# Optimization experiments

Measured on AMD Instinct MI355X. Metric: run time of the kernel, lower is better.

## Reference

```python
import math
import jax, jax.numpy as jnp
import numpy as np

B, N, D_IN, D_OUT = 8, 2048, 768, 768

def setup_inputs() -> dict:
    key = jax.random.key(0)
    k1, k2, k3 = jax.random.split(key, 3)
    x = jax.random.normal(k1, (B, N, D_IN), dtype=jnp.float32)
    W_qkv = jax.random.normal(k2, (D_IN, 3 * D_OUT), dtype=jnp.float32) * (1.0 / math.sqrt(D_IN))
    b_qkv = jax.random.normal(k3, (3 * D_OUT,), dtype=jnp.float32) * 0.02
    return {"x": x, "W_qkv": W_qkv, "b_qkv": b_qkv}

def reference(x, W_qkv, b_qkv):
    d_out = D_OUT
    # fused QKV projection: [B, N, 3*d_out]
    qkv = jnp.einsum('bnd,de->bne', x, W_qkv) + b_qkv
    q = qkv[:, :, :d_out]
    k = qkv[:, :, d_out:2 * d_out]
    v = qkv[:, :, 2 * d_out:3 * d_out]
    scale = 1.0 / math.sqrt(d_out)
    # scores: [B, N, N]
    scores = jnp.einsum('bqd,bkd->bqk', q, k) * scale
    attn = jax.nn.softmax(scores, axis=-1)
    # context: [B, N, d_out]
    context = jnp.einsum('bqk,bkd->bqd', attn, v)
    return context
```

## Files before the change

### kernel.cpp

```cpp
#include <hip/hip_runtime.h>
#include <hip/hip_bf16.h>

typedef __attribute__((ext_vector_type(8))) short short8;
typedef __attribute__((ext_vector_type(4))) float floatx4;

#define BATCH 8
#define SEQ 2048
#define DMODEL 768
#define NQKV 2304
#define SCALE 0.03608439182435161f

__device__ __forceinline__ ushort f2bf(float f) {
    union { float f; uint u; } in; in.f = f;
    uint u = in.u;
    return (ushort)((u + 0x7FFFu + ((u >> 16) & 1u)) >> 16);
}
__device__ __forceinline__ float bf2f(ushort h) {
    union { uint u; float f; } o; o.u = ((uint)h) << 16;
    return o.f;
}

__device__ __forceinline__ void async_copy16(void* lds_uniform, const void* gaddr) {
    __builtin_amdgcn_global_load_lds(
        (const __attribute__((address_space(1))) void*)gaddr,
        (__attribute__((address_space(3))) void*)lds_uniform,
        16, 0, 0);
}

#define BARRIER() asm volatile("s_barrier" ::: "memory")
#define LGKM0()   do { asm volatile("s_waitcnt lgkmcnt(0)" ::: "memory"); \
                       __builtin_amdgcn_sched_barrier(0); } while (0)
#define LGKM_HINT() asm volatile("s_waitcnt lgkmcnt(8)" ::: "memory")
#define VMCNT(n)  asm volatile("s_waitcnt vmcnt(" #n ")" ::: "memory")

template<int MODE, int KT>
__global__ __launch_bounds__(512, 2) void gemm8(
    const ushort* __restrict__ A, const ushort* __restrict__ B,
    const float* __restrict__ bias,
    void* __restrict__ out0, void* __restrict__ out1, void* __restrict__ out2,
    int lda, int ldb)
{
    extern __shared__ __align__(16) ushort lds[];
    const int tid  = threadIdx.x;
    const int w    = tid >> 6, lane = tid & 63;
    const int wr   = w >> 2,  wc   = w & 3;
    const int lr   = lane & 15, kg = lane >> 4;
    const int srow = lane >> 3;
    const int scc  = (lane & 7) ^ srow;

    const int m0 = blockIdx.x * 256, n0 = blockIdx.y * 256;
    const ushort* Abase;
    const ushort* Bbase;
    if (MODE == 0) {
        Abase = A + (size_t)m0 * lda;
        Bbase = B + (size_t)n0 * ldb;
    } else {
        const int b = blockIdx.z;
        Abase = A + ((size_t)(b * SEQ + m0)) * lda;
        Bbase = B + ((size_t)(b * SEQ + n0)) * ldb;
    }

    const ushort* At[2] = { lds,         lds + 32768 };
    const ushort* Bt[2] = { lds + 16384, lds + 49152 };

    #define STG(tile, mat, half) do { if ((tile) < KT) {                          \
        ushort* sb_ = lds + (((tile) & 1) ? 32768 : 0) + ((mat) ? 16384 : 0);     \
        const ushort* g_ = (mat) ? Bbase : Abase;                                 \
        const size_t ld_ = (mat) ? (size_t)ldb : (size_t)lda;                     \
        const int k0_ = (tile) << 6;                                              \
        _Pragma("unroll")                                                         \
        for (int t_ = 0; t_ < 2; ++t_) {                                          \
            const int c8_ = (mat) ? ((w & 3) + ((w >> 2) << 3) + (t_ << 4) + ((half) << 2)) \
                                  : (w + (t_ << 4) + ((half) << 3));              \
            const int row_ = (c8_ << 3) + srow;                                   \
            async_copy16(sb_ + c8_ * 512, g_ + (size_t)row_ * ld_ + k0_ + scc * 8); \
        } } } while (0)

    short8 af[4][2], bf[4][2];
    floatx4 acc[8][4] = {};

    #define LDFRAG(tp, row, c) \
        (*reinterpret_cast<const short8*>(&(tp)[((row) << 6) + ((((c) ^ ((row) & 7))) << 3)]))

    #define READ_A(bufi, mh) do {                                                 \
        _Pragma("unroll") for (int mf_ = 0; mf_ < 4; ++mf_)                       \
        _Pragma("unroll") for (int kk_ = 0; kk_ < 2; ++kk_)                       \
            af[mf_][kk_] = LDFRAG(At[bufi], wr * 128 + ((mh) * 4 + mf_) * 16 + lr, kk_ * 4 + kg); \
    } while (0)
    #define READ_B(bufi, nh) do {                                                 \
        _Pragma("unroll") for (int nf_ = 0; nf_ < 2; ++nf_)                       \
        _Pragma("unroll") for (int kk_ = 0; kk_ < 2; ++kk_)                       \
            bf[(nh) * 2 + nf_][kk_] = LDFRAG(Bt[bufi], wc * 64 + ((nh) * 2 + nf_) * 16 + lr, kk_ * 4 + kg); \
    } while (0)
    #define MFMA_Q(mh, nh) do {                                                   \
        __builtin_amdgcn_s_setprio(1);                                            \
        _Pragma("unroll") for (int mf_ = 0; mf_ < 4; ++mf_)                       \
        _Pragma("unroll") for (int nf_ = 0; nf_ < 2; ++nf_)                       \
        _Pragma("unroll") for (int kk_ = 0; kk_ < 2; ++kk_)                       \
            acc[(mh) * 4 + mf_][(nh) * 2 + nf_] = __builtin_amdgcn_mfma_f32_16x16x32_bf16( \
                af[mf_][kk_], bf[(nh) * 2 + nf_][kk_], acc[(mh) * 4 + mf_][(nh) * 2 + nf_], 0, 0, 0); \
        __builtin_amdgcn_s_setprio(0);                                            \
    } while (0)

    STG(0, 0, 0); STG(0, 1, 0); STG(0, 1, 1); STG(0, 0, 1);
    STG(1, 0, 0); STG(1, 1, 0); STG(1, 1, 1);
    VMCNT(6);
    BARRIER();

    #pragma unroll 1
    for (int it = 0; it < KT / 2; ++it) {
        const int t = 2 * it;
        const bool lastit = (it == KT / 2 - 1);
        READ_A(0, 0); READ_B(0, 0);
        STG(t + 1, 0, 1);
        LGKM_HINT();
        BARRIER(); LGKM0();
        MFMA_Q(0, 0);
        BARRIER();
        READ_B(0, 1);
        STG(t + 2, 0, 0);
        BARRIER(); LGKM0();
        MFMA_Q(0, 1);
        BARRIER();
        READ_A(0, 1);
        STG(t + 2, 1, 0);
        BARRIER(); LGKM0();
        MFMA_Q(1, 0);
        BARRIER();
        STG(t + 2, 1, 1);
        BARRIER();
        MFMA_Q(1, 1);
        if (lastit) { VMCNT(0); } else { VMCNT(6); }
        BARRIER();
        READ_A(1, 0); READ_B(1, 0);
        STG(t + 2, 0, 1);
        LGKM_HINT();
        BARRIER(); LGKM0();
        MFMA_Q(0, 0);
        BARRIER();
        READ_B(1, 1);
        STG(t + 3, 0, 0);
        BARRIER(); LGKM0();
        MFMA_Q(0, 1);
        BARRIER();
        READ_A(1, 1);
        STG(t + 3, 1, 0);
        BARRIER(); LGKM0();
        MFMA_Q(1, 0);
        BARRIER();
        STG(t + 3, 1, 1);
        BARRIER();
        MFMA_Q(1, 1);
        VMCNT(6);
        BARRIER();
    }

    const int mrow = m0 + wr * 128;
    const int ncol = n0 + wc * 64;

    if (MODE == 0 && blockIdx.y >= 6) {
        ushort* Vt = (ushort*)out2;
        const int bIdx = m0 >> 11;
        const int ns0  = m0 & 2047;
        #pragma unroll
        for (int nf = 0; nf < 4; ++nf) {
            const int e = ncol + nf * 16 + lr;
            const int d = e - 2 * DMODEL;
            const float bv = bias[e];
            ushort* vrow = Vt + ((size_t)bIdx * DMODEL + d) * SEQ + ns0;
            #pragma unroll
            for (int a = 0; a < 8; ++a) {
                const floatx4 v = acc[a][nf];
                uint2 u;
                u.x = (uint)f2bf(v[0] + bv) | ((uint)f2bf(v[1] + bv) << 16);
                u.y = (uint)f2bf(v[2] + bv) | ((uint)f2bf(v[3] + bv) << 16);
                *reinterpret_cast<uint2*>(vrow + wr * 128 + a * 16 + kg * 4) = u;
            }
        }
    } else {
        float* scr = reinterpret_cast<float*>(reinterpret_cast<char*>(lds) + (size_t)w * 9216);
        #pragma unroll
        for (int mh = 0; mh < 2; ++mh) {
            #pragma unroll
            for (int np = 0; np < 2; ++np) {
                #pragma unroll
                for (int mf = 0; mf < 4; ++mf)
                    #pragma unroll
                    for (int nf2 = 0; nf2 < 2; ++nf2) {
                        const floatx4 v = acc[mh * 4 + mf][np * 2 + nf2];
                        #pragma unroll
                        for (int r = 0; r < 4; ++r)
                            scr[(mf * 16 + kg * 4 + r) * 36 + nf2 * 16 + lr] = v[r];
                    }
                asm volatile("s_waitcnt lgkmcnt(0)" ::: "memory");
                __builtin_amdgcn_sched_barrier(0);

                const int c8 = (lane & 3) * 8;
                const int e0 = ncol + np * 32 + c8;
                ushort* dst; int ec; float mul;
                float bs[8] = {0, 0, 0, 0, 0, 0, 0, 0};
                if (MODE == 0) {
                    const bool isQ = e0 < DMODEL;
                    dst = isQ ? (ushort*)out0 : (ushort*)out1;
                    ec  = isQ ? e0 : e0 - DMODEL;
                    mul = isQ ? SCALE : 1.0f;
                    const float4 b0 = *reinterpret_cast<const float4*>(&bias[e0]);
                    const float4 b1 = *reinterpret_cast<const float4*>(&bias[e0 + 4]);
                    bs[0] = b0.x * mul; bs[1] = b0.y * mul;
                    bs[2] = b0.z * mul; bs[3] = b0.w * mul;
                    bs[4] = b1.x * mul; bs[5] = b1.y * mul;
                    bs[6] = b1.z * mul; bs[7] = b1.w * mul;
                } else {
                    dst = (ushort*)out0 + (size_t)blockIdx.z * SEQ * SEQ;
                    ec = e0; mul = 1.0f;
                }
                const size_t ostride = (MODE == 0) ? (size_t)DMODEL : (size_t)SEQ;
                #pragma unroll
                for (int p = 0; p < 4; ++p) {
                    const int row = p * 16 + (lane >> 2);
                    const float4 lo = *reinterpret_cast<const float4*>(&scr[row * 36 + c8]);
                    const float4 hi = *reinterpret_cast<const float4*>(&scr[row * 36 + c8 + 4]);
                    short8 o;
                    o[0] = (short)f2bf(lo.x * mul + bs[0]);
                    o[1] = (short)f2bf(lo.y * mul + bs[1]);
                    o[2] = (short)f2bf(lo.z * mul + bs[2]);
                    o[3] = (short)f2bf(lo.w * mul + bs[3]);
                    o[4] = (short)f2bf(hi.x * mul + bs[4]);
                    o[5] = (short)f2bf(hi.y * mul + bs[5]);
                    o[6] = (short)f2bf(hi.z * mul + bs[6]);
                    o[7] = (short)f2bf(hi.w * mul + bs[7]);
                    *reinterpret_cast<short8*>(
                        &dst[(size_t)(mrow + mh * 64 + row) * ostride + ec]) = o;
                }
                asm volatile("s_waitcnt lgkmcnt(0)" ::: "memory");
                __builtin_amdgcn_sched_barrier(0);
            }
        }
    }
    #undef STG
    #undef LDFRAG
    #undef READ_A
    #undef READ_B
    #undef MFMA_Q
}

__global__ __launch_bounds__(512, 4) void pv128(
    const ushort* __restrict__ P, const ushort* __restrict__ V,
    float* __restrict__ Out)
{
    extern __shared__ __align__(16) ushort lds[];
    const int tid  = threadIdx.x;
    const int w    = tid >> 6, lane = tid & 63;
    const int wr   = w >> 2,  wc   = w & 3;
    const int lr   = lane & 15, kg = lane >> 4;
    const int srow = lane >> 3;
    const int scc  = (lane & 7) ^ srow;

    const int m0 = blockIdx.x * 128, n0 = blockIdx.y * 192;
    const int b  = blockIdx.z;
    const ushort* Abase = P + (size_t)b * SEQ * SEQ + (size_t)m0 * SEQ;
    const ushort* Bbase = V + (size_t)b * DMODEL * SEQ + (size_t)n0 * SEQ;

    const ushort* At[2] = { lds,         lds + 8192 };
    const ushort* Bt[2] = { lds + 16384, lds + 28672 };
    const int KT = 32;

    #define STG_A(tile, half) do { if ((tile) < KT) {                             \
        ushort* sb_ = lds + (((tile) & 1) ? 8192 : 0);                            \
        const int k0_ = (tile) << 6;                                              \
        const int c8_ = (w & 3) + ((w >> 2) << 3) + ((half) << 2);                \
        const int row_ = (c8_ << 3) + srow;                                       \
        async_copy16(sb_ + c8_ * 512, Abase + (size_t)row_ * SEQ + k0_ + scc * 8); \
    } } while (0)
    #define STG_B0(tile) do { if ((tile) < KT) {                                  \
        ushort* sb_ = lds + 16384 + (((tile) & 1) ? 12288 : 0);                   \
        const int k0_ = (tile) << 6;                                              \
        _Pragma("unroll")                                                         \
        for (int t_ = 0; t_ < 2; ++t_) {                                          \
            const int idx_ = w * 2 + t_;                                          \
            const int c8_ = (idx_ >> 2) * 6 + (idx_ & 3);                         \
            const int row_ = (c8_ << 3) + srow;                                   \
            async_copy16(sb_ + c8_ * 512, Bbase + (size_t)row_ * SEQ + k0_ + scc * 8); \
        } } } while (0)
    #define STG_B1(tile) do { if ((tile) < KT) {                                  \
        ushort* sb_ = lds + 16384 + (((tile) & 1) ? 12288 : 0);                   \
        const int k0_ = (tile) << 6;                                              \
        const int c8_ = (w >> 1) * 6 + 4 + (w & 1);                               \
        const int row_ = (c8_ << 3) + srow;                                       \
        async_copy16(sb_ + c8_ * 512, Bbase + (size_t)row_ * SEQ + k0_ + scc * 8); \
    } } while (0)

    short8 af[2][2], bf[3][2];
    floatx4 acc[4][3] = {};

    #define LDFRAG(tp, row, c) \
        (*reinterpret_cast<const short8*>(&(tp)[((row) << 6) + ((((c) ^ ((row) & 7))) << 3)]))

    #define READ_A(bufi, mh) do {                                                 \
        _Pragma("unroll") for (int mf_ = 0; mf_ < 2; ++mf_)                       \
        _Pragma("unroll") for (int kk_ = 0; kk_ < 2; ++kk_)                       \
            af[mf_][kk_] = LDFRAG(At[bufi], wr * 64 + ((mh) * 2 + mf_) * 16 + lr, kk_ * 4 + kg); \
    } while (0)
    #define READ_B_N0(bufi) do {                                                  \
        _Pragma("unroll") for (int nf_ = 0; nf_ < 2; ++nf_)                       \
        _Pragma("unroll") for (int kk_ = 0; kk_ < 2; ++kk_)                       \
            bf[nf_][kk_] = LDFRAG(Bt[bufi], wc * 48 + nf_ * 16 + lr, kk_ * 4 + kg); \
    } while (0)
    #define READ_B_N1(bufi) do {                                                  \
        _Pragma("unroll") for (int kk_ = 0; kk_ < 2; ++kk_)                       \
            bf[2][kk_] = LDFRAG(Bt[bufi], wc * 48 + 32 + lr, kk_ * 4 + kg);       \
    } while (0)
    #define MFMA_N0(mh) do {                                                      \
        __builtin_amdgcn_s_setprio(1);                                            \
        _Pragma("unroll") for (int mf_ = 0; mf_ < 2; ++mf_)                       \
        _Pragma("unroll") for (int nf_ = 0; nf_ < 2; ++nf_)                       \
        _Pragma("unroll") for (int kk_ = 0; kk_ < 2; ++kk_)                       \
            acc[(mh) * 2 + mf_][nf_] = __builtin_amdgcn_mfma_f32_16x16x32_bf16(   \
                af[mf_][kk_], bf[nf_][kk_], acc[(mh) * 2 + mf_][nf_], 0, 0, 0);   \
        __builtin_amdgcn_s_setprio(0);                                            \
    } while (0)
    #define MFMA_N1(mh) do {                                                      \
        __builtin_amdgcn_s_setprio(1);                                            \
        _Pragma("unroll") for (int mf_ = 0; mf_ < 2; ++mf_)                       \
        _Pragma("unroll") for (int kk_ = 0; kk_ < 2; ++kk_)                       \
            acc[(mh) * 2 + mf_][2] = __builtin_amdgcn_mfma_f32_16x16x32_bf16(     \
                af[mf_][kk_], bf[2][kk_], acc[(mh) * 2 + mf_][2], 0, 0, 0);       \
        __builtin_amdgcn_s_setprio(0);                                            \
    } while (0)

    STG_A(0, 0); STG_B0(0); STG_B1(0); STG_A(0, 1);
    STG_A(1, 0); STG_B0(1); STG_B1(1);
    VMCNT(4);
    BARRIER();

    #pragma unroll 1
    for (int it = 0; it < KT / 2; ++it) {
        const int t = 2 * it;
        const bool lastit = (it == KT / 2 - 1);
        READ_A(0, 0); READ_B_N0(0);
        STG_A(t + 1, 1);
        BARRIER(); LGKM0();
        MFMA_N0(0);
        BARRIER();
        READ_B_N1(0);
        STG_A(t + 2, 0);
        BARRIER(); LGKM0();
        MFMA_N1(0);
        BARRIER();
        READ_A(0, 1);
        STG_B0(t + 2);
        BARRIER(); LGKM0();
        MFMA_N0(1);
        BARRIER();
        STG_B1(t + 2);
        BARRIER();
        MFMA_N1(1);
        if (lastit) { VMCNT(0); } else { VMCNT(4); }
        BARRIER();
        READ_A(1, 0); READ_B_N0(1);
        STG_A(t + 2, 1);
        BARRIER(); LGKM0();
        MFMA_N0(0);
        BARRIER();
        READ_B_N1(1);
        STG_A(t + 3, 0);
        BARRIER(); LGKM0();
        MFMA_N1(0);
        BARRIER();
        READ_A(1, 1);
        STG_B0(t + 3);
        BARRIER(); LGKM0();
        MFMA_N0(1);
        BARRIER();
        STG_B1(t + 3);
        BARRIER();
        MFMA_N1(1);
        VMCNT(4);
        BARRIER();
    }

    const int mrow = m0 + wr * 64;
    const int ncol = n0 + wc * 48;
    float* scr = reinterpret_cast<float*>(reinterpret_cast<char*>(lds) + (size_t)w * 5120);
    float* Ob = Out + (size_t)b * SEQ * DMODEL;
    #pragma unroll
    for (int np = 0; np < 3; ++np) {
        #pragma unroll
        for (int mf = 0; mf < 4; ++mf) {
            const floatx4 v = acc[mf][np];
            #pragma unroll
            for (int r = 0; r < 4; ++r)
                scr[(mf * 16 + kg * 4 + r) * 20 + lr] = v[r];
        }
        asm volatile("s_waitcnt lgkmcnt(0)" ::: "memory");
        __builtin_amdgcn_sched_barrier(0);

        const int c4 = (lane & 3) * 4;
        #pragma unroll
        for (int p = 0; p < 4; ++p) {
            const int row = p * 16 + (lane >> 2);
            const float4 v = *reinterpret_cast<const float4*>(&scr[row * 20 + c4]);
            *reinterpret_cast<float4*>(
                &Ob[(size_t)(mrow + row) * DMODEL + ncol + np * 16 + c4]) = v;
        }
        asm volatile("s_waitcnt lgkmcnt(0)" ::: "memory");
        __builtin_amdgcn_sched_barrier(0);
    }
    #undef STG_A
    #undef STG_B0
    #undef STG_B1
    #undef LDFRAG
    #undef READ_A
    #undef READ_B_N0
    #undef READ_B_N1
    #undef MFMA_N0
    #undef MFMA_N1
}

__global__ __launch_bounds__(256) void qkv_vtail(
    const ushort* __restrict__ Xb,
    const ushort* __restrict__ Wt,
    const float* __restrict__ bias,
    ushort* __restrict__ Vt)
{
    __shared__ __align__(16) ushort smem[2 * 128 * 32];
    ushort* As = smem;
    ushort* Bs = smem + 128 * 32;
    const int tid  = threadIdx.x;
    const int m0   = blockIdx.x * 128;
    const int n0   = 2048 + blockIdx.y * 128;
    const int wave = tid >> 6, lane = tid & 63;
    const int wm   = (wave >> 1) * 64, wn = (wave & 1) * 64;
    const int lr   = lane & 15, kg = lane >> 4;
    const ushort* Abase = Xb + (size_t)m0 * DMODEL;
    const ushort* Bbase = Wt + (size_t)n0 * DMODEL;
    floatx4 acc[4][4] = {};

    for (int k0 = 0; k0 < DMODEL; k0 += 32) {
        #pragma unroll
        for (int t = 0; t < 2; ++t) {
            const int chunk = wave * 2 + t;
            const int row = chunk * 16 + (lane >> 2);
            async_copy16(As + chunk * 512,
                         Abase + (size_t)row * DMODEL + k0 + (lane & 3) * 8);
        }
        #pragma unroll
        for (int t = 0; t < 2; ++t) {
            const int chunk = wave * 2 + t;
            const int row = chunk * 16 + (lane >> 2);
            async_copy16(Bs + chunk * 512,
                         Bbase + (size_t)row * DMODEL + k0 + (lane & 3) * 8);
        }
        __syncthreads();
        short8 a[4], b[4];
        #pragma unroll
        for (int i = 0; i < 4; ++i)
            a[i] = *reinterpret_cast<const short8*>(&As[(wm + i * 16 + lr) * 32 + kg * 8]);
        #pragma unroll
        for (int j = 0; j < 4; ++j)
            b[j] = *reinterpret_cast<const short8*>(&Bs[(wn + j * 16 + lr) * 32 + kg * 8]);
        #pragma unroll
        for (int i = 0; i < 4; ++i)
            #pragma unroll
            for (int j = 0; j < 4; ++j)
                acc[i][j] = __builtin_amdgcn_mfma_f32_16x16x32_bf16(a[i], b[j], acc[i][j], 0, 0, 0);
        __syncthreads();
    }

    const int bIdx = m0 >> 11;
    const int ns0  = m0 & 2047;
    #pragma unroll
    for (int j = 0; j < 4; ++j) {
        const int e = n0 + wn + j * 16 + lr;
        const int d = e - 2 * DMODEL;
        const float bv = bias[e];
        ushort* vrow = Vt + ((size_t)bIdx * DMODEL + d) * SEQ + ns0;
        #pragma unroll
        for (int i = 0; i < 4; ++i) {
            const floatx4 v = acc[i][j];
            uint2 u;
            u.x = (uint)f2bf(v[0] + bv) | ((uint)f2bf(v[1] + bv) << 16);
            u.y = (uint)f2bf(v[2] + bv) | ((uint)f2bf(v[3] + bv) << 16);
            *reinterpret_cast<uint2*>(vrow + wm + i * 16 + kg * 4) = u;
        }
    }
}

__global__ __launch_bounds__(256) void convert_x(const float* __restrict__ X,
                                                 ushort* __restrict__ Xb) {
    const int total = (BATCH * SEQ * DMODEL) / 8;
    for (int i = blockIdx.x * 256 + threadIdx.x; i < total; i += gridDim.x * 256) {
        const float4 v0 = reinterpret_cast<const float4*>(X)[(size_t)i * 2];
        const float4 v1 = reinterpret_cast<const float4*>(X)[(size_t)i * 2 + 1];
        uint4 u;
        u.x = (uint)f2bf(v0.x) | ((uint)f2bf(v0.y) << 16);
        u.y = (uint)f2bf(v0.z) | ((uint)f2bf(v0.w) << 16);
        u.z = (uint)f2bf(v1.x) | ((uint)f2bf(v1.y) << 16);
        u.w = (uint)f2bf(v1.z) | ((uint)f2bf(v1.w) << 16);
        reinterpret_cast<uint4*>(Xb)[i] = u;
    }
}

__global__ __launch_bounds__(256) void convert_wt(const float* __restrict__ W,
                                                  ushort* __restrict__ Wt) {
    __shared__ float tile[32][33];
    const int n0 = blockIdx.x * 32, k0 = blockIdx.y * 32;
    const int tx = threadIdx.x & 31, ty = threadIdx.x >> 5;
    #pragma unroll
    for (int i = 0; i < 32; i += 8)
        tile[ty + i][tx] = W[(size_t)(k0 + ty + i) * NQKV + n0 + tx];
    __syncthreads();
    #pragma unroll
    for (int i = 0; i < 32; i += 8)
        Wt[(size_t)(n0 + ty + i) * DMODEL + k0 + tx] = f2bf(tile[tx][ty + i]);
}

__global__ __launch_bounds__(256) void softmax_rows(ushort* __restrict__ S) {
    const int row = blockIdx.x;
    ushort* p = S + (size_t)row * SEQ;
    const int tid = threadIdx.x;
    const int wave = tid >> 6, lane = tid & 63;

    short8 v8 = *reinterpret_cast<const short8*>(p + tid * 8);
    float v[8];
    #pragma unroll
    for (int j = 0; j < 8; ++j) v[j] = bf2f((ushort)v8[j]);
    float mx = v[0];
    #pragma unroll
    for (int j = 1; j < 8; ++j) mx = fmaxf(mx, v[j]);
    #pragma unroll
    for (int off = 32; off >= 1; off >>= 1) mx = fmaxf(mx, __shfl_xor(mx, off));
    __shared__ float redm[4], reds[4];
    if (lane == 0) redm[wave] = mx;
    __syncthreads();
    mx = fmaxf(fmaxf(redm[0], redm[1]), fmaxf(redm[2], redm[3]));

    float e[8], s = 0.f;
    #pragma unroll
    for (int j = 0; j < 8; ++j) { e[j] = __expf(v[j] - mx); s += e[j]; }
    #pragma unroll
    for (int off = 32; off >= 1; off >>= 1) s += __shfl_xor(s, off);
    if (lane == 0) reds[wave] = s;
    __syncthreads();
    s = reds[0] + reds[1] + reds[2] + reds[3];
    float inv = 1.f / s;

    short8 o;
    #pragma unroll
    for (int j = 0; j < 8; ++j) o[j] = (short)f2bf(e[j] * inv);
    *reinterpret_cast<short8*>(p + tid * 8) = o;
}

extern "C" void kernel_launch(void* const* d_in, const int* in_sizes, int n_in,
                              void* d_out, int out_size, void* d_ws, size_t ws_size,
                              hipStream_t stream) {
    const float* X    = (const float*)d_in[0];
    const float* W    = (const float*)d_in[1];
    const float* bias = (const float*)d_in[2];
    float* Out = (float*)d_out;

    char* ws = (char*)d_ws;
    ushort* S  = (ushort*)ws;
    ushort* Xb = (ushort*)ws;
    ushort* Wt = (ushort*)(ws + (size_t)BATCH * SEQ * DMODEL * 2);
    ushort* Qs = (ushort*)(ws + (size_t)BATCH * SEQ * SEQ * 2);
    ushort* Kb = Qs + (size_t)BATCH * SEQ * DMODEL;
    ushort* Vt = Kb + (size_t)BATCH * SEQ * DMODEL;

    const int LDSB = 131072;
    (void)hipFuncSetAttribute((const void*)gemm8<0, 12>,
                              hipFuncAttributeMaxDynamicSharedMemorySize, LDSB);
    (void)hipFuncSetAttribute((const void*)gemm8<1, 12>,
                              hipFuncAttributeMaxDynamicSharedMemorySize, LDSB);
    (void)hipFuncSetAttribute((const void*)pv128,
                              hipFuncAttributeMaxDynamicSharedMemorySize, 81920);

    convert_x<<<2048, 256, 0, stream>>>(X, Xb);
    convert_wt<<<dim3(NQKV / 32, DMODEL / 32), 256, 0, stream>>>(W, Wt);
    gemm8<0, 12><<<dim3(64, 8), 512, LDSB, stream>>>(
        Xb, Wt, bias, Qs, Kb, Vt, DMODEL, DMODEL);
    qkv_vtail<<<dim3(128, 2), 256, 0, stream>>>(Xb, Wt, bias, Vt);
    gemm8<1, 12><<<dim3(8, 8, 8), 512, LDSB, stream>>>(
        Qs, Kb, nullptr, S, nullptr, nullptr, DMODEL, DMODEL);
    softmax_rows<<<BATCH * SEQ, 256, 0, stream>>>(S);
    pv128<<<dim3(16, 4, 8), 512, 81920, stream>>>(S, Vt, Out);
}
```

Before: 247.6 us.

## Fuse softmax exponentiation into PV GEMM using per-row log-sum-exp offsets

The softmax kernel now only computes a per-row max plus log-sum-exp offset and no longer writes normalized probabilities back to S. The PV kernel applies exp(s - offset) to the A fragments after loading them from LDS and before the MFMAs. This removes one full bf16 write pass over the 8x2048x2048 score matrix. The cost is that exp is recomputed in the GEMM inner loop, once for each of the 4 column blocks, which adds VALU work that may contend with the MFMA pipeline.

```diff
diff --git a/kernel.cpp b/kernel.cpp
--- a/kernel.cpp
+++ b/kernel.cpp
@@ -244,8 +244,9 @@
     #undef MFMA_Q
 }
 
-__global__ __launch_bounds__(512, 4) void pv128(
+__global__ __launch_bounds__(512, 4) void pv_fused(
     const ushort* __restrict__ P, const ushort* __restrict__ V,
+    const float* __restrict__ Off,
     float* __restrict__ Out)
 {
     extern __shared__ __align__(16) ushort lds[];
@@ -260,6 +261,11 @@
     const int b  = blockIdx.z;
     const ushort* Abase = P + (size_t)b * SEQ * SEQ + (size_t)m0 * SEQ;
     const ushort* Bbase = V + (size_t)b * DMODEL * SEQ + (size_t)n0 * SEQ;
+
+    float off_[4];
+    #pragma unroll
+    for (int i = 0; i < 4; ++i)
+        off_[i] = Off[(size_t)b * SEQ + m0 + wr * 64 + i * 16 + lr];
 
     const ushort* At[2] = { lds,         lds + 8192 };
     const ushort* Bt[2] = { lds + 16384, lds + 28672 };
@@ -301,6 +307,15 @@
         _Pragma("unroll") for (int kk_ = 0; kk_ < 2; ++kk_)                       \
             af[mf_][kk_] = LDFRAG(At[bufi], wr * 64 + ((mh) * 2 + mf_) * 16 + lr, kk_ * 4 + kg); \
     } while (0)
+    #define SMX(mh) do {                                                          \
+        _Pragma("unroll") for (int mf_ = 0; mf_ < 2; ++mf_) {                     \
+            const float o_ = off_[(mh) * 2 + mf_];                                \
+            _Pragma("unroll") for (int kk_ = 0; kk_ < 2; ++kk_)                   \
+            _Pragma("unroll") for (int j_ = 0; j_ < 8; ++j_)                      \
+                af[mf_][kk_][j_] = (short)f2bf(                                   \
+                    __expf(bf2f((ushort)af[mf_][kk_][j_]) - o_));                 \
+        }                                                                         \
+    } while (0)
     #define READ_B_N0(bufi) do {                                                  \
         _Pragma("unroll") for (int nf_ = 0; nf_ < 2; ++nf_)                       \
         _Pragma("unroll") for (int kk_ = 0; kk_ < 2; ++kk_)                       \
@@ -340,6 +355,7 @@
         READ_A(0, 0); READ_B_N0(0);
         STG_A(t + 1, 1);
         BARRIER(); LGKM0();
+        SMX(0);
         MFMA_N0(0);
         BARRIER();
         READ_B_N1(0);
@@ -350,6 +366,7 @@
         READ_A(0, 1);
         STG_B0(t + 2);
         BARRIER(); LGKM0();
+        SMX(1);
         MFMA_N0(1);
         BARRIER();
         STG_B1(t + 2);
@@ -360,6 +377,7 @@
         READ_A(1, 0); READ_B_N0(1);
         STG_A(t + 2, 1);
         BARRIER(); LGKM0();
+        SMX(0);
         MFMA_N0(0);
         BARRIER();
         READ_B_N1(1);
@@ -370,6 +388,7 @@
         READ_A(1, 1);
         STG_B0(t + 3);
         BARRIER(); LGKM0();
+        SMX(1);
         MFMA_N0(1);
         BARRIER();
         STG_B1(t + 3);
@@ -411,6 +430,7 @@
     #undef STG_B1
     #undef LDFRAG
     #undef READ_A
+    #undef SMX
     #undef READ_B_N0
     #undef READ_B_N1
     #undef MFMA_N0
@@ -515,9 +535,10 @@
         Wt[(size_t)(n0 + ty + i) * DMODEL + k0 + tx] = f2bf(tile[tx][ty + i]);
 }
 
-__global__ __launch_bounds__(256) void softmax_rows(ushort* __restrict__ S) {
+__global__ __launch_bounds__(256) void row_stats(const ushort* __restrict__ S,
+                                                 float* __restrict__ Off) {
     const int row = blockIdx.x;
-    ushort* p = S + (size_t)row * SEQ;
+    const ushort* p = S + (size_t)row * SEQ;
     const int tid = threadIdx.x;
     const int wave = tid >> 6, lane = tid & 63;
 
@@ -535,20 +556,17 @@
     __syncthreads();
     mx = fmaxf(fmaxf(redm[0], redm[1]), fmaxf(redm[2], redm[3]));
 
-    float e[8], s = 0.f;
-    #pragma unroll
-    for (int j = 0; j < 8; ++j) { e[j] = __expf(v[j] - mx); s += e[j]; }
+    float s = 0.f;
+    #pragma unroll
+    for (int j = 0; j < 8; ++j) s += __expf(v[j] - mx);
     #pragma unroll
     for (int off = 32; off >= 1; off >>= 1) s += __shfl_xor(s, off);
     if (lane == 0) reds[wave] = s;
     __syncthreads();
-    s = reds[0] + reds[1] + reds[2] + reds[3];
-    float inv = 1.f / s;
-
-    short8 o;
-    #pragma unroll
-    for (int j = 0; j < 8; ++j) o[j] = (short)f2bf(e[j] * inv);
-    *reinterpret_cast<short8*>(p + tid * 8) = o;
+    if (tid == 0) {
+        s = reds[0] + reds[1] + reds[2] + reds[3];
+        Off[row] = mx + __logf(s);
+    }
 }
 
 extern "C" void kernel_launch(void* const* d_in, const int* in_sizes, int n_in,
@@ -566,13 +584,14 @@
     ushort* Qs = (ushort*)(ws + (size_t)BATCH * SEQ * SEQ * 2);
     ushort* Kb = Qs + (size_t)BATCH * SEQ * DMODEL;
     ushort* Vt = Kb + (size_t)BATCH * SEQ * DMODEL;
+    float*  Off = (float*)(Vt + (size_t)BATCH * SEQ * DMODEL);
 
     const int LDSB = 131072;
     (void)hipFuncSetAttribute((const void*)gemm8<0, 12>,
                               hipFuncAttributeMaxDynamicSharedMemorySize, LDSB);
     (void)hipFuncSetAttribute((const void*)gemm8<1, 12>,
                               hipFuncAttributeMaxDynamicSharedMemorySize, LDSB);
-    (void)hipFuncSetAttribute((const void*)pv128,
+    (void)hipFuncSetAttribute((const void*)pv_fused,
                               hipFuncAttributeMaxDynamicSharedMemorySize, 81920);
 
     convert_x<<<2048, 256, 0, stream>>>(X, Xb);
@@ -582,6 +601,6 @@
     qkv_vtail<<<dim3(128, 2), 256, 0, stream>>>(Xb, Wt, bias, Vt);
     gemm8<1, 12><<<dim3(8, 8, 8), 512, LDSB, stream>>>(
         Qs, Kb, nullptr, S, nullptr, nullptr, DMODEL, DMODEL);
-    softmax_rows<<<BATCH * SEQ, 256, 0, stream>>>(S);
-    pv128<<<dim3(16, 4, 8), 512, 81920, stream>>>(S, Vt, Out);
-}
+    row_stats<<<BATCH * SEQ, 256, 0, stream>>>(S, Off);
+    pv_fused<<<dim3(16, 4, 8), 512, 81920, stream>>>(S, Vt, Off, Out);
+}
```

Result: slower. 378.7 us (+53.0%).
